# Optimization experiments

Hardware: AMD Instinct MI355X
Metric: run time of the kernel (lower is better)

Reference implementation:

```python
import jax, jax.numpy as jnp
import numpy as np

DIM = 384
HEADS = 12
WS = 7
MLPH = 1536
B = 32
EPS = 1e-5


def _rel_index():
    coords = np.stack(np.meshgrid(np.arange(WS), np.arange(WS), indexing='ij'))  # [2,7,7]
    cf = coords.reshape(2, -1)  # [2,49]
    rel = cf[:, :, None] - cf[:, None, :]  # [2,49,49]
    rel = rel.transpose(1, 2, 0).astype(np.int64)
    rel[:, :, 0] += WS - 1
    rel[:, :, 1] += WS - 1
    rel[:, :, 0] *= 2 * WS - 1
    return jnp.asarray(rel.sum(-1), dtype=jnp.int32)  # [49,49]


def setup_inputs() -> dict:
    key = jax.random.key(0)
    ks = jax.random.split(key, 16)
    H, W = 56, 56
    L = H * W
    s = 0.02
    inp = {
        'x': jax.random.normal(ks[0], (B, L, DIM), jnp.float32),
        'ln1_g': jnp.ones((DIM,), jnp.float32),
        'ln1_b': jnp.zeros((DIM,), jnp.float32),
        'qkv_w': jax.random.normal(ks[1], (DIM, 3 * DIM), jnp.float32) * s,
        'qkv_b': jnp.zeros((3 * DIM,), jnp.float32),
        'rpb_table': jax.random.normal(ks[2], ((2 * WS - 1) ** 2, HEADS), jnp.float32) * s,
        'proj_w': jax.random.normal(ks[3], (DIM, DIM), jnp.float32) * s,
        'proj_b': jnp.zeros((DIM,), jnp.float32),
        'ln2_g': jnp.ones((DIM,), jnp.float32),
        'ln2_b': jnp.zeros((DIM,), jnp.float32),
        'mlp_w1': jax.random.normal(ks[4], (DIM, MLPH), jnp.float32) * s,
        'mlp_b1': jnp.zeros((MLPH,), jnp.float32),
        'mlp_w2': jax.random.normal(ks[5], (MLPH, DIM), jnp.float32) * s,
        'mlp_b2': jnp.zeros((DIM,), jnp.float32),
        'rel_idx': _rel_index(),
        'H': H,
        'W': W,
    }
    return inp


def _ln(x, g, b):
    m = jnp.mean(x, axis=-1, keepdims=True)
    v = jnp.mean(jnp.square(x - m), axis=-1, keepdims=True)
    return (x - m) * jax.lax.rsqrt(v + EPS) * g + b


def reference(x, ln1_g, ln1_b, qkv_w, qkv_b, rpb_table, proj_w, proj_b,
              ln2_g, ln2_b, mlp_w1, mlp_b1, mlp_w2, mlp_b2, rel_idx, H, W):
    Bb, L, C = x.shape
    N = WS * WS
    hd = C // HEADS
    scale = hd ** -0.5

    shortcut = x
    h = _ln(x, ln1_g, ln1_b).reshape(Bb, H, W, C)
    # window partition -> [nW, 49, C]
    h = h.reshape(Bb, H // WS, WS, W // WS, WS, C).transpose(0, 1, 3, 2, 4, 5)
    wins = h.reshape(-1, N, C)
    nW = wins.shape[0]

    qkv = (wins @ qkv_w + qkv_b).reshape(nW, N, 3, HEADS, hd).transpose(2, 0, 3, 1, 4)
    q, k, v = qkv[0] * scale, qkv[1], qkv[2]  # [nW, heads, 49, hd]

    attn = jnp.einsum('bhnd,bhmd->bhnm', q, k)
    bias = rpb_table[rel_idx].transpose(2, 0, 1)  # [heads,49,49]
    attn = jax.nn.softmax(attn + bias[None], axis=-1)
    out = jnp.einsum('bhnm,bhmd->bhnd', attn, v).transpose(0, 2, 1, 3).reshape(nW, N, C)
    out = out @ proj_w + proj_b

    # window reverse -> [B, L, C]
    out = out.reshape(Bb, H // WS, W // WS, WS, WS, C).transpose(0, 1, 3, 2, 4, 5).reshape(Bb, L, C)

    x = shortcut + out
    h2 = _ln(x, ln2_g, ln2_b)
    mlp = jax.nn.gelu(h2 @ mlp_w1 + mlp_b1, approximate=False) @ mlp_w2 + mlp_b2
    return x + mlp
```

## Files before the change

### kernel.cpp

```cpp
#include <hip/hip_runtime.h>
#include <hip/hip_bf16.h>
#include <cstdint>
#include <cstddef>

#define HEADS 12
#define LL 3136
#define ROWS 100352
#define SCALE 0.17677669529663687f

typedef __hip_bfloat16 bf16;
typedef __attribute__((ext_vector_type(8))) short short8;
typedef __attribute__((ext_vector_type(4))) short s4;
typedef __attribute__((ext_vector_type(4))) float f32x4;

__device__ __forceinline__ float bf2f(unsigned short u) {
  union { uint32_t u32; float f; } x; x.u32 = ((uint32_t)u) << 16; return x.f;
}
__device__ __forceinline__ unsigned short f2bf_bits(float f) {
  union { float f; uint32_t u; } x; x.f = f;
  uint32_t r = x.u + 0x7fffu + ((x.u >> 16) & 1u);
  return (unsigned short)(r >> 16);
}
__device__ __forceinline__ float gelu_fast(float x) {
  float t2 = x * (1.5957691216f + 0.0713548162726f * x * x);
  float e = __expf(t2);
  return x * (e / (e + 1.0f) );
}

__global__ __launch_bounds__(64) void prep_fragB(const float* __restrict__ src,
    bf16* __restrict__ dst, int K, int N, int scaleLim, float scale) {
  const int nf = blockIdx.x, kf = blockIdx.y;
  const int l = threadIdx.x;
  const int n = nf * 16 + (l & 15);
  const int k0 = kf * 32 + (l >> 4) * 8;
  const float sc = (n < scaleLim) ? scale : 1.f;
  short8 v;
  #pragma unroll
  for (int j = 0; j < 8; ++j)
    v[j] = (short)f2bf_bits(src[(size_t)(k0 + j) * N + n] * sc);
  *(short8*)&dst[(((size_t)nf * (K >> 5) + kf) * 64 + l) * 8] = v;
}

__global__ void prep_qb(const float* __restrict__ qkv_b, float* __restrict__ qb) {
  int idx = blockIdx.x * 256 + threadIdx.x;
  if (idx < 1152) qb[idx] = qkv_b[idx] * (idx < 384 ? SCALE : 1.0f);
}

__global__ void prep_biasM(const float* __restrict__ rpb, const int* __restrict__ rel,
                           f32x4* __restrict__ biasM) {
  int h = blockIdx.x;
  int t = blockIdx.y;
  int mi = t >> 2, ni = t & 3;
  int lane = threadIdx.x;
  int q = ni * 16 + (lane & 15);
  int g = lane >> 4;
  f32x4 v;
  #pragma unroll
  for (int j = 0; j < 4; ++j) {
    int k = mi * 16 + g * 4 + j;
    float b;
    if (k < 49) b = (q < 49) ? rpb[rel[q * 49 + k] * HEADS + h] : 0.f;
    else        b = -1e30f;
    v[j] = b;
  }
  biasM[((h * 4 + mi) * 4 + ni) * 64 + lane] = v;
}

template<bool WIN, bool BF16IN>
__global__ __launch_bounds__(256) void ln_kernel(const float* __restrict__ xf,
    const bf16* __restrict__ xb, const float* __restrict__ g,
    const float* __restrict__ b, bf16* __restrict__ out) {
  int row = blockIdx.x * 4 + (threadIdx.x >> 6);
  int lane = threadIdx.x & 63;
  size_t src;
  if (WIN) {
    int w = row / 49, p = row - w * 49;
    int bb = w >> 6, wy = (w >> 3) & 7, wx = w & 7;
    int iy = p / 7, ix = p - iy * 7;
    int l = (wy * 7 + iy) * 56 + wx * 7 + ix;
    src = ((size_t)bb * LL + l) * 384;
  } else {
    src = (size_t)row * 384;
  }
  float vals[6];
  float s = 0.f, s2 = 0.f;
  #pragma unroll
  for (int j = 0; j < 6; ++j) {
    float v = BF16IN ? bf2f(*(const unsigned short*)&xb[src + lane + 64 * j])
                     : xf[src + lane + 64 * j];
    vals[j] = v; s += v; s2 += v * v;
  }
  #pragma unroll
  for (int off = 32; off >= 1; off >>= 1) {
    s  += __shfl_xor(s, off);
    s2 += __shfl_xor(s2, off);
  }
  float m  = s * (1.f / 384.f);
  float var = s2 * (1.f / 384.f) - m * m;
  float rs = rsqrtf(var + 1e-5f);
  bf16* orow = out + (size_t)row * 384;
  #pragma unroll
  for (int j = 0; j < 6; ++j) {
    int c = lane + 64 * j;
    orow[c] = __float2bfloat16((vals[j] - m) * rs * g[c] + b[c]);
  }
}

template<int EPI>
__global__ __launch_bounds__(256) void gemm_bt(const bf16* __restrict__ A,
    const bf16* __restrict__ Bt, const float* __restrict__ bias,
    bf16* __restrict__ Cb, float* __restrict__ Cf, const float* __restrict__ resid,
    const bf16* __restrict__ residb, int M, int N, int K) {
  __shared__ bf16 lsA[2][128 * 32];
  const int t = threadIdx.x;
  const int lane = t & 63;
  const int wave = t >> 6;
  const int wm = wave >> 1, wn = wave & 1;
  const int lrow = lane & 15;
  const int lk = (lane >> 4) * 8;
  const int nbx = N >> 7;
  const int nwg = (M >> 7) * nbx;
  const int cpx = nwg >> 3;
  const int id2 = (blockIdx.x & 7) * cpx + (blockIdx.x >> 3);
  const int n0 = (id2 % nbx) * 128;
  const int m0 = (id2 / nbx) * 128;
  const int nkf = K >> 5;

  f32x4 acc[4][4];
  #pragma unroll
  for (int i = 0; i < 4; ++i)
    #pragma unroll
    for (int j = 0; j < 4; ++j) acc[i][j] = (f32x4){0.f, 0.f, 0.f, 0.f};

  auto stageA = [&](int buf, int tile) {
    int k0 = tile * 32;
    #pragma unroll
    for (int i = 0; i < 2; ++i) {
      int e = (i * 256 + t) * 8;
      int r = e >> 5, c = e & 31;
      const bf16* ga = A + (size_t)(m0 + r) * K + (k0 + c);
      __builtin_amdgcn_global_load_lds((const __attribute__((address_space(1))) void*)ga,
          (__attribute__((address_space(3))) void*)&lsA[buf][e], 16, 0, 0);
    }
  };

  auto loadB = [&](int kf, short8 (&dst)[4]) {
    const bf16* fb = Bt + (((size_t)((n0 >> 4) + wn * 4) * nkf + kf) * 64 + lane) * 8;
    #pragma unroll
    for (int ni = 0; ni < 4; ++ni)
      dst[ni] = *(const short8*)(fb + (size_t)ni * nkf * 512);
  };

  auto computeA = [&](int buf, const short8 (&bfr)[4]) {
    short8 af[4];
    #pragma unroll
    for (int mi = 0; mi < 4; ++mi)
      af[mi] = *(const short8*)&lsA[buf][(wm * 64 + mi * 16 + lrow) * 32 + lk];
    #pragma unroll
    for (int mi = 0; mi < 4; ++mi)
      #pragma unroll
      for (int ni = 0; ni < 4; ++ni)
        acc[mi][ni] = __builtin_amdgcn_mfma_f32_16x16x32_bf16(af[mi], bfr[ni], acc[mi][ni], 0, 0, 0);
  };

  const int nt = K >> 5;
  short8 b0[4], b1[4];
  stageA(0, 0);
  loadB(0, b0);
  __syncthreads();
  int cur = 0;
  for (int it = 0; it < nt; ++it) {
    if (it + 1 < nt) {
      stageA(cur ^ 1, it + 1);
      loadB(it + 1, b1);
    }
    computeA(cur, b0);
    __syncthreads();
    if (it + 1 < nt) {
      #pragma unroll
      for (int i = 0; i < 4; ++i) b0[i] = b1[i];
    }
    cur ^= 1;
  }

  #pragma unroll
  for (int mi = 0; mi < 4; ++mi) {
    #pragma unroll
    for (int ni = 0; ni < 4; ++ni) {
      int col = n0 + wn * 64 + ni * 16 + lrow;
      float bv = bias[col];
      #pragma unroll
      for (int j = 0; j < 4; ++j) {
        int row = m0 + wm * 64 + mi * 16 + (lane >> 4) * 4 + j;
        float v = acc[mi][ni][j] + bv;
        if constexpr (EPI == 0) {
          Cb[(size_t)row * N + col] = __float2bfloat16(v);
        } else if constexpr (EPI == 1) {
          Cb[(size_t)row * N + col] = __float2bfloat16(gelu_fast(v));
        } else if constexpr (EPI == 2) {
          int w = row / 49, p = row - w * 49;
          int bb = w >> 6, wy = (w >> 3) & 7, wx = w & 7;
          int iy = p / 7, ix = p - iy * 7;
          int l = (wy * 7 + iy) * 56 + wx * 7 + ix;
          size_t di = ((size_t)bb * LL + l) * 384 + col;
          Cb[di] = __float2bfloat16(v + resid[di]);
        } else {
          size_t di = (size_t)row * N + col;
          Cf[di] = v + bf2f(*(const unsigned short*)&residb[di]);
        }
      }
    }
  }
}

__global__ __launch_bounds__(256) void attn_mfma(const bf16* __restrict__ qkv,
    const f32x4* __restrict__ biasM, bf16* __restrict__ out) {
  __shared__ __align__(16) short lds4[4][6272];
  const int wv = threadIdx.x >> 6;
  const int lane = threadIdx.x & 63;
  const int w = blockIdx.x * 4 + wv;
  const int h = blockIdx.y;
  short* L = &lds4[wv][0];
  const short* base = (const short*)(qkv + (size_t)w * 49 * 1152 + h * 32);

  #pragma unroll
  for (int i = 0; i < 4; ++i) {
    int t = i * 64 + lane;
    int r = t >> 2, c = t & 3;
    short8 qv, kv, vv;
    if (r < 49) {
      const short* rp = base + (size_t)r * 1152;
      qv = *(const short8*)(rp + c * 8);
      kv = *(const short8*)(rp + 384 + c * 8);
      vv = *(const short8*)(rp + 768 + c * 8);
    } else {
      qv = (short8)0; kv = (short8)0; vv = (short8)0;
    }
    *(short8*)&L[r * 32 + c * 8] = kv;
    *(short8*)&L[2048 + r * 32 + c * 8] = qv;
    #pragma unroll
    for (int j = 0; j < 8; ++j) L[4096 + (c * 8 + j) * 68 + r] = vv[j];
  }

  const int g = lane >> 4, r15 = lane & 15;

  short8 ka[4], qb[4];
  #pragma unroll
  for (int mi = 0; mi < 4; ++mi)
    ka[mi] = *(const short8*)&L[(mi * 16 + r15) * 32 + g * 8];
  #pragma unroll
  for (int ni = 0; ni < 4; ++ni)
    qb[ni] = *(const short8*)&L[2048 + (ni * 16 + r15) * 32 + g * 8];

  f32x4 sT[4][4];
  #pragma unroll
  for (int mi = 0; mi < 4; ++mi)
    #pragma unroll
    for (int ni = 0; ni < 4; ++ni)
      sT[mi][ni] = biasM[((h * 4 + mi) * 4 + ni) * 64 + lane];
  #pragma unroll
  for (int mi = 0; mi < 4; ++mi)
    #pragma unroll
    for (int ni = 0; ni < 4; ++ni)
      sT[mi][ni] = __builtin_amdgcn_mfma_f32_16x16x32_bf16(ka[mi], qb[ni], sT[mi][ni], 0, 0, 0);

  float inv_[4];
  #pragma unroll
  for (int ni = 0; ni < 4; ++ni) {
    float m = -1e30f;
    #pragma unroll
    for (int mi = 0; mi < 4; ++mi)
      #pragma unroll
      for (int j = 0; j < 4; ++j) m = fmaxf(m, sT[mi][ni][j]);
    m = fmaxf(m, __shfl_xor(m, 16));
    m = fmaxf(m, __shfl_xor(m, 32));
    float s = 0.f;
    #pragma unroll
    for (int mi = 0; mi < 4; ++mi)
      #pragma unroll
      for (int j = 0; j < 4; ++j) {
        float p = __expf(sT[mi][ni][j] - m);
        sT[mi][ni][j] = p; s += p;
      }
    s += __shfl_xor(s, 16);
    s += __shfl_xor(s, 32);
    inv_[ni] = 1.f / s;
  }

  s4 pa[4][4];
  #pragma unroll
  for (int mi = 0; mi < 4; ++mi)
    #pragma unroll
    for (int ni = 0; ni < 4; ++ni) {
      s4 p;
      #pragma unroll
      for (int j = 0; j < 4; ++j)
        p[j] = (short)f2bf_bits(sT[mi][ni][j] * inv_[ni]);
      pa[mi][ni] = p;
    }

  s4 vb[4][2];
  #pragma unroll
  for (int mi = 0; mi < 4; ++mi)
    #pragma unroll
    for (int di = 0; di < 2; ++di)
      vb[mi][di] = *(const s4*)&L[4096 + (di * 16 + r15) * 68 + mi * 16 + g * 4];

  f32x4 o[4][2];
  #pragma unroll
  for (int ni = 0; ni < 4; ++ni)
    #pragma unroll
    for (int di = 0; di < 2; ++di) o[ni][di] = (f32x4){0.f, 0.f, 0.f, 0.f};

  asm volatile("s_nop 3" ::: );
  #pragma unroll
  for (int ni = 0; ni < 4; ++ni)
    #pragma unroll
    for (int di = 0; di < 2; ++di)
      #pragma unroll
      for (int mi = 0; mi < 4; ++mi) {
#if __has_builtin(__builtin_amdgcn_mfma_f32_16x16x16bf16_1k)
        o[ni][di] = __builtin_amdgcn_mfma_f32_16x16x16bf16_1k(pa[mi][ni], vb[mi][di], o[ni][di], 0, 0, 0);
#else
        asm volatile("v_mfma_f32_16x16x16_bf16 %0, %1, %2, %0"
                     : "+v"(o[ni][di]) : "v"(pa[mi][ni]), "v"(vb[mi][di]));
#endif
      }
  asm volatile("s_nop 7\n\ts_nop 7" ::: );

  bf16* op = out + ((size_t)w * 49) * 384 + h * 32;
  #pragma unroll
  for (int ni = 0; ni < 4; ++ni)
    #pragma unroll
    for (int di = 0; di < 2; ++di)
      #pragma unroll
      for (int j = 0; j < 4; ++j) {
        int q = ni * 16 + g * 4 + j;
        if (q < 49)
          op[(size_t)q * 384 + di * 16 + r15] = __float2bfloat16(o[ni][di][j]);
      }
}

extern "C" void kernel_launch(void* const* d_in, const int* in_sizes, int n_in,
                              void* d_out, int out_size, void* d_ws, size_t ws_size,
                              hipStream_t stream) {
  const float* x      = (const float*)d_in[0];
  const float* ln1_g  = (const float*)d_in[1];
  const float* ln1_b  = (const float*)d_in[2];
  const float* qkv_w  = (const float*)d_in[3];
  const float* qkv_b  = (const float*)d_in[4];
  const float* rpb    = (const float*)d_in[5];
  const float* proj_w = (const float*)d_in[6];
  const float* proj_b = (const float*)d_in[7];
  const float* ln2_g  = (const float*)d_in[8];
  const float* ln2_b  = (const float*)d_in[9];
  const float* mlp_w1 = (const float*)d_in[10];
  const float* mlp_b1 = (const float*)d_in[11];
  const float* mlp_w2 = (const float*)d_in[12];
  const float* mlp_b2 = (const float*)d_in[13];
  const int*   rel    = (const int*)d_in[14];

  char* ws = (char*)d_ws;
  const size_t OFF_WQKV  = 0;
  const size_t OFF_WPROJ = OFF_WQKV + (size_t)1152 * 384 * 2;
  const size_t OFF_WM1   = OFF_WPROJ + (size_t)384 * 384 * 2;
  const size_t OFF_WM2   = OFF_WM1 + (size_t)1536 * 384 * 2;
  const size_t OFF_QB    = OFF_WM2 + (size_t)384 * 1536 * 2;
  const size_t OFF_HWIN  = 3659776;
  const size_t OFF_QKV   = OFF_HWIN + (size_t)ROWS * 384 * 2;
  const size_t OFF_ATTN  = OFF_QKV + (size_t)ROWS * 1152 * 2;
  const size_t OFF_X2    = OFF_ATTN + (size_t)ROWS * 384 * 2;
  const size_t OFF_M1    = OFF_QKV;
  const size_t OFF_H2    = OFF_HWIN;
  const size_t OFF_BIASM = OFF_X2 + (size_t)ROWS * 384 * 2;

  bf16*  wqkv  = (bf16*)(ws + OFF_WQKV);
  bf16*  wproj = (bf16*)(ws + OFF_WPROJ);
  bf16*  wm1   = (bf16*)(ws + OFF_WM1);
  bf16*  wm2   = (bf16*)(ws + OFF_WM2);
  float* qb    = (float*)(ws + OFF_QB);
  f32x4* biasM = (f32x4*)(ws + OFF_BIASM);
  bf16*  hwin  = (bf16*)(ws + OFF_HWIN);
  bf16*  qkvb  = (bf16*)(ws + OFF_QKV);
  bf16*  attnb = (bf16*)(ws + OFF_ATTN);
  bf16*  x2b   = (bf16*)(ws + OFF_X2);
  bf16*  m1    = (bf16*)(ws + OFF_M1);
  bf16*  h2    = (bf16*)(ws + OFF_H2);
  float* outp  = (float*)d_out;

  prep_fragB<<<dim3(1152 / 16, 384 / 32), 64, 0, stream>>>(qkv_w, wqkv, 384, 1152, 384, SCALE);
  prep_fragB<<<dim3(384 / 16, 384 / 32), 64, 0, stream>>>(proj_w, wproj, 384, 384, 0, 1.f);
  prep_fragB<<<dim3(1536 / 16, 384 / 32), 64, 0, stream>>>(mlp_w1, wm1, 384, 1536, 0, 1.f);
  prep_fragB<<<dim3(384 / 16, 1536 / 32), 64, 0, stream>>>(mlp_w2, wm2, 1536, 384, 0, 1.f);
  prep_qb<<<5, 256, 0, stream>>>(qkv_b, qb);
  prep_biasM<<<dim3(12, 16), 64, 0, stream>>>(rpb, rel, biasM);

  ln_kernel<true, false><<<ROWS / 4, 256, 0, stream>>>(x, nullptr, ln1_g, ln1_b, hwin);
  gemm_bt<0><<<(1152 / 128) * (ROWS / 128), 256, 0, stream>>>(
      hwin, wqkv, qb, qkvb, nullptr, nullptr, nullptr, ROWS, 1152, 384);
  attn_mfma<<<dim3(512, HEADS), 256, 0, stream>>>(qkvb, biasM, attnb);
  gemm_bt<2><<<(384 / 128) * (ROWS / 128), 256, 0, stream>>>(
      attnb, wproj, proj_b, x2b, nullptr, x, nullptr, ROWS, 384, 384);
  ln_kernel<false, true><<<ROWS / 4, 256, 0, stream>>>(nullptr, x2b, ln2_g, ln2_b, h2);
  gemm_bt<1><<<(1536 / 128) * (ROWS / 128), 256, 0, stream>>>(
      h2, wm1, mlp_b1, m1, nullptr, nullptr, nullptr, ROWS, 1536, 384);
  gemm_bt<3><<<(384 / 128) * (ROWS / 128), 256, 0, stream>>>(
      m1, wm2, mlp_b2, nullptr, outp, nullptr, x2b, ROWS, 384, 1536);
}
```

Measured before the change: 938.3 us.

## Stage full 384-wide A K-chunk in LDS instead of double-buffered 32-wide tiles

The GEMM now loads a whole 128x384 A chunk into LDS (96 KB) in one pass, syncs once, then runs all MFMA k-steps from LDS. This replaces the per-32-column double-buffered loop that needed a barrier per k-step. It also makes K a compile-time template parameter. In exchange, the larger LDS footprint cuts occupancy to about one block per CU, and there is no overlap between loading A and computing within a chunk. B fragments are now loaded synchronously right before use with no prefetch.

```diff
diff --git a/kernel.cpp b/kernel.cpp
--- a/kernel.cpp
+++ b/kernel.cpp
@@ -24,7 +24,7 @@
 __device__ __forceinline__ float gelu_fast(float x) {
   float t2 = x * (1.5957691216f + 0.0713548162726f * x * x);
   float e = __expf(t2);
-  return x * (e / (e + 1.0f) );
+  return x * (e / (e + 1.0f));
 }
 
 __global__ __launch_bounds__(64) void prep_fragB(const float* __restrict__ src,
@@ -106,12 +106,16 @@
   }
 }
 
-template<int EPI>
+template<int EPI, int KTOT>
 __global__ __launch_bounds__(256) void gemm_bt(const bf16* __restrict__ A,
     const bf16* __restrict__ Bt, const float* __restrict__ bias,
     bf16* __restrict__ Cb, float* __restrict__ Cf, const float* __restrict__ resid,
-    const bf16* __restrict__ residb, int M, int N, int K) {
-  __shared__ bf16 lsA[2][128 * 32];
+    const bf16* __restrict__ residb, int M, int N) {
+  constexpr int KC  = 384;
+  constexpr int NCH = KTOT / KC;
+  constexpr int NT  = KC / 32;
+  constexpr int NKF = KTOT >> 5;
+  __shared__ bf16 lsA[128 * KC];
   const int t = threadIdx.x;
   const int lane = t & 63;
   const int wave = t >> 6;
@@ -124,7 +128,6 @@
   const int id2 = (blockIdx.x & 7) * cpx + (blockIdx.x >> 3);
   const int n0 = (id2 % nbx) * 128;
   const int m0 = (id2 / nbx) * 128;
-  const int nkf = K >> 5;
 
   f32x4 acc[4][4];
   #pragma unroll
@@ -132,55 +135,38 @@
     #pragma unroll
     for (int j = 0; j < 4; ++j) acc[i][j] = (f32x4){0.f, 0.f, 0.f, 0.f};
 
-  auto stageA = [&](int buf, int tile) {
-    int k0 = tile * 32;
-    #pragma unroll
-    for (int i = 0; i < 2; ++i) {
-      int e = (i * 256 + t) * 8;
-      int r = e >> 5, c = e & 31;
-      const bf16* ga = A + (size_t)(m0 + r) * K + (k0 + c);
-      __builtin_amdgcn_global_load_lds((const __attribute__((address_space(1))) void*)ga,
-          (__attribute__((address_space(3))) void*)&lsA[buf][e], 16, 0, 0);
-    }
-  };
-
-  auto loadB = [&](int kf, short8 (&dst)[4]) {
-    const bf16* fb = Bt + (((size_t)((n0 >> 4) + wn * 4) * nkf + kf) * 64 + lane) * 8;
-    #pragma unroll
-    for (int ni = 0; ni < 4; ++ni)
-      dst[ni] = *(const short8*)(fb + (size_t)ni * nkf * 512);
-  };
-
-  auto computeA = [&](int buf, const short8 (&bfr)[4]) {
-    short8 af[4];
-    #pragma unroll
-    for (int mi = 0; mi < 4; ++mi)
-      af[mi] = *(const short8*)&lsA[buf][(wm * 64 + mi * 16 + lrow) * 32 + lk];
-    #pragma unroll
-    for (int mi = 0; mi < 4; ++mi)
+  for (int kc = 0; kc < NCH; ++kc) {
+    if (kc) __syncthreads();
+    #pragma unroll
+    for (int tt = 0; tt < NT; ++tt) {
+      #pragma unroll
+      for (int i = 0; i < 2; ++i) {
+        int e = (i * 256 + t) * 8;
+        int r = e >> 5, c = e & 31;
+        const bf16* ga = A + (size_t)(m0 + r) * KTOT + kc * KC + tt * 32 + c;
+        __builtin_amdgcn_global_load_lds((const __attribute__((address_space(1))) void*)ga,
+            (__attribute__((address_space(3))) void*)&lsA[tt * 4096 + e], 16, 0, 0);
+      }
+    }
+    __syncthreads();
+    #pragma unroll
+    for (int tt = 0; tt < NT; ++tt) {
+      const int kf = kc * NT + tt;
+      short8 bfr[4];
+      const bf16* fb = Bt + (((size_t)((n0 >> 4) + wn * 4) * NKF + kf) * 64 + lane) * 8;
       #pragma unroll
       for (int ni = 0; ni < 4; ++ni)
-        acc[mi][ni] = __builtin_amdgcn_mfma_f32_16x16x32_bf16(af[mi], bfr[ni], acc[mi][ni], 0, 0, 0);
-  };
-
-  const int nt = K >> 5;
-  short8 b0[4], b1[4];
-  stageA(0, 0);
-  loadB(0, b0);
-  __syncthreads();
-  int cur = 0;
-  for (int it = 0; it < nt; ++it) {
-    if (it + 1 < nt) {
-      stageA(cur ^ 1, it + 1);
-      loadB(it + 1, b1);
-    }
-    computeA(cur, b0);
-    __syncthreads();
-    if (it + 1 < nt) {
-      #pragma unroll
-      for (int i = 0; i < 4; ++i) b0[i] = b1[i];
-    }
-    cur ^= 1;
+        bfr[ni] = *(const short8*)(fb + (size_t)ni * NKF * 512);
+      short8 af[4];
+      #pragma unroll
+      for (int mi = 0; mi < 4; ++mi)
+        af[mi] = *(const short8*)&lsA[tt * 4096 + (wm * 64 + mi * 16 + lrow) * 32 + lk];
+      #pragma unroll
+      for (int mi = 0; mi < 4; ++mi)
+        #pragma unroll
+        for (int ni = 0; ni < 4; ++ni)
+          acc[mi][ni] = __builtin_amdgcn_mfma_f32_16x16x32_bf16(af[mi], bfr[ni], acc[mi][ni], 0, 0, 0);
+    }
   }
 
   #pragma unroll
@@ -396,14 +382,14 @@
   prep_biasM<<<dim3(12, 16), 64, 0, stream>>>(rpb, rel, biasM);
 
   ln_kernel<true, false><<<ROWS / 4, 256, 0, stream>>>(x, nullptr, ln1_g, ln1_b, hwin);
-  gemm_bt<0><<<(1152 / 128) * (ROWS / 128), 256, 0, stream>>>(
-      hwin, wqkv, qb, qkvb, nullptr, nullptr, nullptr, ROWS, 1152, 384);
+  gemm_bt<0, 384><<<(1152 / 128) * (ROWS / 128), 256, 0, stream>>>(
+      hwin, wqkv, qb, qkvb, nullptr, nullptr, nullptr, ROWS, 1152);
   attn_mfma<<<dim3(512, HEADS), 256, 0, stream>>>(qkvb, biasM, attnb);
-  gemm_bt<2><<<(384 / 128) * (ROWS / 128), 256, 0, stream>>>(
-      attnb, wproj, proj_b, x2b, nullptr, x, nullptr, ROWS, 384, 384);
+  gemm_bt<2, 384><<<(384 / 128) * (ROWS / 128), 256, 0, stream>>>(
+      attnb, wproj, proj_b, x2b, nullptr, x, nullptr, ROWS, 384);
   ln_kernel<false, true><<<ROWS / 4, 256, 0, stream>>>(nullptr, x2b, ln2_g, ln2_b, h2);
-  gemm_bt<1><<<(1536 / 128) * (ROWS / 128), 256, 0, stream>>>(
-      h2, wm1, mlp_b1, m1, nullptr, nullptr, nullptr, ROWS, 1536, 384);
-  gemm_bt<3><<<(384 / 128) * (ROWS / 128), 256, 0, stream>>>(
-      m1, wm2, mlp_b2, nullptr, outp, nullptr, x2b, ROWS, 384, 1536);
-}
+  gemm_bt<1, 384><<<(1536 / 128) * (ROWS / 128), 256, 0, stream>>>(
+      h2, wm1, mlp_b1, m1, nullptr, nullptr, nullptr, ROWS, 1536);
+  gemm_bt<3, 1536><<<(384 / 128) * (ROWS / 128), 256, 0, stream>>>(
+      m1, wm2, mlp_b2, nullptr, outp, nullptr, x2b, ROWS, 384);
+}
```

New measurement: 1.073 ms. +14.4%, slower.

## Widen GEMM tiles to 128x384 with 12 waves sharing each A tile

Applied to the files above, without the earlier changes.

The GEMM block tile grows from 128x128 with 4 waves to 128x384 with 12 waves (2x6 wave grid), so every staged A tile in LDS feeds three times as many columns and A is read from global memory fewer times. The K dimension becomes a template constant so loop bounds and B-fragment strides are known at compile time. The trade-off is a 768-thread block with one barrier across all 12 waves, fewer blocks overall, and only 512 of the 768 threads doing A staging. Per-wave register use is unchanged, but each block is larger, which may change occupancy and scheduling.

```diff
diff --git a/kernel.cpp b/kernel.cpp
--- a/kernel.cpp
+++ b/kernel.cpp
@@ -24,7 +24,7 @@
 __device__ __forceinline__ float gelu_fast(float x) {
   float t2 = x * (1.5957691216f + 0.0713548162726f * x * x);
   float e = __expf(t2);
-  return x * (e / (e + 1.0f) );
+  return x * (e / (e + 1.0f));
 }
 
 __global__ __launch_bounds__(64) void prep_fragB(const float* __restrict__ src,
@@ -106,25 +106,26 @@
   }
 }
 
-template<int EPI>
-__global__ __launch_bounds__(256) void gemm_bt(const bf16* __restrict__ A,
+template<int EPI, int KTOT>
+__global__ __launch_bounds__(768) void gemm_bt(const bf16* __restrict__ A,
     const bf16* __restrict__ Bt, const float* __restrict__ bias,
     bf16* __restrict__ Cb, float* __restrict__ Cf, const float* __restrict__ resid,
-    const bf16* __restrict__ residb, int M, int N, int K) {
+    const bf16* __restrict__ residb, int M, int N) {
+  constexpr int NKF = KTOT >> 5;
   __shared__ bf16 lsA[2][128 * 32];
   const int t = threadIdx.x;
   const int lane = t & 63;
   const int wave = t >> 6;
-  const int wm = wave >> 1, wn = wave & 1;
+  const int wm = wave / 6;
+  const int wn = wave % 6;
   const int lrow = lane & 15;
   const int lk = (lane >> 4) * 8;
-  const int nbx = N >> 7;
+  const int nbx = N / 384;
   const int nwg = (M >> 7) * nbx;
   const int cpx = nwg >> 3;
   const int id2 = (blockIdx.x & 7) * cpx + (blockIdx.x >> 3);
-  const int n0 = (id2 % nbx) * 128;
+  const int n0 = (id2 % nbx) * 384;
   const int m0 = (id2 / nbx) * 128;
-  const int nkf = K >> 5;
 
   f32x4 acc[4][4];
   #pragma unroll
@@ -133,22 +134,20 @@
     for (int j = 0; j < 4; ++j) acc[i][j] = (f32x4){0.f, 0.f, 0.f, 0.f};
 
   auto stageA = [&](int buf, int tile) {
-    int k0 = tile * 32;
-    #pragma unroll
-    for (int i = 0; i < 2; ++i) {
-      int e = (i * 256 + t) * 8;
+    if (t < 512) {
+      int e = t * 8;
       int r = e >> 5, c = e & 31;
-      const bf16* ga = A + (size_t)(m0 + r) * K + (k0 + c);
+      const bf16* ga = A + (size_t)(m0 + r) * KTOT + tile * 32 + c;
       __builtin_amdgcn_global_load_lds((const __attribute__((address_space(1))) void*)ga,
           (__attribute__((address_space(3))) void*)&lsA[buf][e], 16, 0, 0);
     }
   };
 
   auto loadB = [&](int kf, short8 (&dst)[4]) {
-    const bf16* fb = Bt + (((size_t)((n0 >> 4) + wn * 4) * nkf + kf) * 64 + lane) * 8;
+    const bf16* fb = Bt + (((size_t)((n0 >> 4) + wn * 4) * NKF + kf) * 64 + lane) * 8;
     #pragma unroll
     for (int ni = 0; ni < 4; ++ni)
-      dst[ni] = *(const short8*)(fb + (size_t)ni * nkf * 512);
+      dst[ni] = *(const short8*)(fb + (size_t)ni * NKF * 512);
   };
 
   auto computeA = [&](int buf, const short8 (&bfr)[4]) {
@@ -163,7 +162,7 @@
         acc[mi][ni] = __builtin_amdgcn_mfma_f32_16x16x32_bf16(af[mi], bfr[ni], acc[mi][ni], 0, 0, 0);
   };
 
-  const int nt = K >> 5;
+  const int nt = KTOT >> 5;
   short8 b0[4], b1[4];
   stageA(0, 0);
   loadB(0, b0);
@@ -396,14 +395,14 @@
   prep_biasM<<<dim3(12, 16), 64, 0, stream>>>(rpb, rel, biasM);
 
   ln_kernel<true, false><<<ROWS / 4, 256, 0, stream>>>(x, nullptr, ln1_g, ln1_b, hwin);
-  gemm_bt<0><<<(1152 / 128) * (ROWS / 128), 256, 0, stream>>>(
-      hwin, wqkv, qb, qkvb, nullptr, nullptr, nullptr, ROWS, 1152, 384);
+  gemm_bt<0, 384><<<(ROWS / 128) * (1152 / 384), 768, 0, stream>>>(
+      hwin, wqkv, qb, qkvb, nullptr, nullptr, nullptr, ROWS, 1152);
   attn_mfma<<<dim3(512, HEADS), 256, 0, stream>>>(qkvb, biasM, attnb);
-  gemm_bt<2><<<(384 / 128) * (ROWS / 128), 256, 0, stream>>>(
-      attnb, wproj, proj_b, x2b, nullptr, x, nullptr, ROWS, 384, 384);
+  gemm_bt<2, 384><<<(ROWS / 128) * (384 / 384), 768, 0, stream>>>(
+      attnb, wproj, proj_b, x2b, nullptr, x, nullptr, ROWS, 384);
   ln_kernel<false, true><<<ROWS / 4, 256, 0, stream>>>(nullptr, x2b, ln2_g, ln2_b, h2);
-  gemm_bt<1><<<(1536 / 128) * (ROWS / 128), 256, 0, stream>>>(
-      h2, wm1, mlp_b1, m1, nullptr, nullptr, nullptr, ROWS, 1536, 384);
-  gemm_bt<3><<<(384 / 128) * (ROWS / 128), 256, 0, stream>>>(
-      m1, wm2, mlp_b2, nullptr, outp, nullptr, x2b, ROWS, 384, 1536);
-}
+  gemm_bt<1, 384><<<(ROWS / 128) * (1536 / 384), 768, 0, stream>>>(
+      h2, wm1, mlp_b1, m1, nullptr, nullptr, nullptr, ROWS, 1536);
+  gemm_bt<3, 1536><<<(ROWS / 128) * (384 / 384), 768, 0, stream>>>(
+      m1, wm2, mlp_b2, nullptr, outp, nullptr, x2b, ROWS, 384);
+}
```

After: 986.2 us. 1.05x slower.
